# Kernel optimization log

Measured on AMD Instinct MI355X. Metric: run time of the kernel, lower is better.

## Reference

```python
import jax, jax.numpy as jnp
import numpy as np

D = 512
SCALE = 1.0 / np.sqrt(D).astype(np.float32)


def setup_inputs() -> dict:
    key = jax.random.key(0)
    ks = jax.random.split(key, 6)
    B, S = 8, 2048
    x = jax.random.normal(ks[0], (B, S, D), dtype=jnp.float32)
    bias = jax.random.normal(ks[1], (1,), dtype=jnp.float32)
    key_padding_mask = jax.random.randint(ks[2], (B, S), 0, 2).astype(jnp.bool_)
    # nn.Linear weights, stored as [out, in]; y = x @ W.T
    Wq = jax.random.normal(ks[3], (D, D), dtype=jnp.float32) * (1.0 / np.sqrt(D))
    Wk = jax.random.normal(ks[4], (D, D), dtype=jnp.float32) * (1.0 / np.sqrt(D))
    Wv = jax.random.normal(ks[5], (D, D), dtype=jnp.float32) * (1.0 / np.sqrt(D))
    return {"x": x, "bias": bias, "key_padding_mask": key_padding_mask,
            "Wq": Wq, "Wk": Wk, "Wv": Wv}


def reference(x, bias, key_padding_mask, Wq, Wk, Wv):
    # Projections (Linear without bias): [B,S,D] @ [D,D]^T
    Q = jnp.einsum('bsd,ed->bse', x, Wq)
    K = jnp.einsum('bsd,ed->bse', x, Wk)
    V = jnp.einsum('bsd,ed->bse', x, Wv)
    # Scaled scores with additive scalar bias: [B,S,S]
    scores = jnp.einsum('bqd,bkd->bqk', Q, K) * SCALE + bias
    # Key padding mask: mask keys (last dim) with -inf
    scores = jnp.where(key_padding_mask[:, None, :], -jnp.inf, scores)
    attn = jax.nn.softmax(scores, axis=-1)
    attn = jnp.nan_to_num(attn, nan=0.0)  # fully-masked rows -> 0
    # Dropout is inference no-op
    return jnp.einsum('bqk,bkd->bqd', attn, V)
```

## Files before the change

### kernel.cpp

```cpp
#include <hip/hip_runtime.h>

typedef short bf16x8 __attribute__((ext_vector_type(8)));
typedef float f32x4 __attribute__((ext_vector_type(4)));
typedef float f32x16 __attribute__((ext_vector_type(16)));

__device__ __forceinline__ ushort f2bf(float f) {
    union { float f; unsigned u; } v; v.f = f;
    unsigned r = (v.u + 0x7fffu + ((v.u >> 16) & 1u)) >> 16;
    return (ushort)r;
}
__device__ __forceinline__ float bf2f(ushort u) {
    union { unsigned u; float f; } v; v.u = ((unsigned)u) << 16;
    return v.f;
}
__device__ __forceinline__ void async_copy16(void* lds, const void* g) {
    __builtin_amdgcn_global_load_lds(
        (const __attribute__((address_space(1))) unsigned*)g,
        (__attribute__((address_space(3))) unsigned*)lds, 16, 0, 0);
}
__device__ __forceinline__ void lds_barrier() {
    asm volatile("s_waitcnt lgkmcnt(0)\n\ts_barrier" ::: "memory");
}

__global__ __launch_bounds__(256)
void prep_kernel(const float* __restrict__ x, const float* __restrict__ Wq,
                 const float* __restrict__ Wk, const float* __restrict__ Wv,
                 const int* __restrict__ mask,
                 ushort* __restrict__ xb, ushort* __restrict__ wqT,
                 ushort* __restrict__ wkT, ushort* __restrict__ wvb,
                 int* __restrict__ idx, int* __restrict__ cnt)
{
    const int bid = blockIdx.x, t = threadIdx.x;
    if (bid < 8192) {
        int i = (bid * 256 + t) * 4;
        float4 v = *(const float4*)(x + i);
        ushort4 o;
        o.x = f2bf(v.x); o.y = f2bf(v.y); o.z = f2bf(v.z); o.w = f2bf(v.w);
        *(ushort4*)(xb + i) = o;
    } else if (bid < 8320) {
        __shared__ ushort T[64][72];
        int r = bid - 8192;
        const int z = r >> 6; r &= 63;
        const float* in = z ? Wk : Wq;
        ushort* out     = z ? wkT : wqT;
        const int r0 = (r >> 3) * 64, c0 = (r & 7) * 64;
        const int rr = t >> 3, cc8 = (t & 7) * 8;
        #pragma unroll
        for (int pass = 0; pass < 2; ++pass) {
            int rw = rr + pass * 32;
            float4 a = *(const float4*)(in + (size_t)(r0 + rw) * 512 + c0 + cc8);
            float4 bq = *(const float4*)(in + (size_t)(r0 + rw) * 512 + c0 + cc8 + 4);
            T[rw][cc8+0]=f2bf(a.x);  T[rw][cc8+1]=f2bf(a.y);  T[rw][cc8+2]=f2bf(a.z);  T[rw][cc8+3]=f2bf(a.w);
            T[rw][cc8+4]=f2bf(bq.x); T[rw][cc8+5]=f2bf(bq.y); T[rw][cc8+6]=f2bf(bq.z); T[rw][cc8+7]=f2bf(bq.w);
        }
        __syncthreads();
        const int c = t >> 2, seg = (t & 3) * 16;
        ushort tmp[16];
        #pragma unroll
        for (int j = 0; j < 16; ++j) tmp[j] = T[seg + j][c];
        *(uint4*)(out + (size_t)(c0 + c) * 512 + r0 + seg)     = *(uint4*)&tmp[0];
        *(uint4*)(out + (size_t)(c0 + c) * 512 + r0 + seg + 8) = *(uint4*)&tmp[8];
    } else if (bid < 8576) {
        int i = ((bid - 8320) * 256 + t) * 4;
        float4 v = *(const float4*)(Wv + i);
        ushort4 o;
        o.x = f2bf(v.x); o.y = f2bf(v.y); o.z = f2bf(v.z); o.w = f2bf(v.w);
        *(ushort4*)(wvb + i) = o;
    } else {
        __shared__ int sc[256];
        int seg = bid - 8576, b = seg >> 1, half = seg & 1;
        const int* m = mask + b * 2048 + half * 1024;
        int v0 = (m[t*4+0] == 0), v1 = (m[t*4+1] == 0);
        int v2 = (m[t*4+2] == 0), v3 = (m[t*4+3] == 0);
        int c = v0 + v1 + v2 + v3;
        sc[t] = c; __syncthreads();
        for (int ofs = 1; ofs < 256; ofs <<= 1) {
            int xx = (t >= ofs) ? sc[t - ofs] : 0;
            __syncthreads(); sc[t] += xx; __syncthreads();
        }
        int pos = sc[t] - c + seg * 1024;
        if (v0) idx[pos++] = t*4+0;
        if (v1) idx[pos++] = t*4+1;
        if (v2) idx[pos++] = t*4+2;
        if (v3) idx[pos++] = t*4+3;
        if (t == 255) cnt[seg] = sc[255];
    }
}

__global__ __launch_bounds__(256)
void gather_cvt(const float* __restrict__ x, const int* __restrict__ idx,
                const int* __restrict__ cnt, ushort* __restrict__ xc)
{
    int seg = blockIdx.x, b = seg >> 1, half = seg & 1;
    int n = cnt[seg];
    int wave = threadIdx.x >> 6, lane = threadIdx.x & 63;
    int j0 = blockIdx.y * 64 + wave * 16;
    for (int i = 0; i < 16; ++i) {
        int j = j0 + i;
        uint4 val = {0u, 0u, 0u, 0u};
        if (j < n) {
            int src = idx[seg * 1024 + j];
            const float* r = x + ((size_t)(b * 2048 + half * 1024 + src)) * 512 + lane * 8;
            float4 a = *(const float4*)r, c4 = *(const float4*)(r + 4);
            ushort tmp[8];
            tmp[0]=f2bf(a.x); tmp[1]=f2bf(a.y); tmp[2]=f2bf(a.z); tmp[3]=f2bf(a.w);
            tmp[4]=f2bf(c4.x); tmp[5]=f2bf(c4.y); tmp[6]=f2bf(c4.z); tmp[7]=f2bf(c4.w);
            val = *(uint4*)tmp;
        }
        *(uint4*)(xc + ((size_t)(seg * 1024 + j)) * 512 + lane * 8) = val;
    }
}

__device__ __forceinline__ void gemm_core(const ushort* __restrict__ A,
                                          const ushort* __restrict__ B,
                                          ushort* __restrict__ C,
                                          int N, int K, int mBase, int nBase)
{
    __shared__ ushort As[128][32];
    __shared__ ushort Bs[128][32];
    const int tid = threadIdx.x;
    const int lane = tid & 63, wave = tid >> 6;
    const int wm = wave >> 1, wn = wave & 1;
    const int lr = lane & 15, lq = lane >> 4;
    const int sr = lane >> 2;
    const int sc = (lane & 3) * 8;

    f32x4 acc[4][4];
    #pragma unroll
    for (int i = 0; i < 4; ++i)
        #pragma unroll
        for (int j = 0; j < 4; ++j) acc[i][j] = (f32x4){0.f, 0.f, 0.f, 0.f};

    for (int k0 = 0; k0 < K; k0 += 32) {
        __syncthreads();
        #pragma unroll
        for (int j = 0; j < 2; ++j) {
            int rbase = wave * 32 + j * 16;
            async_copy16(&As[rbase][0], A + (size_t)(mBase + rbase + sr) * K + k0 + sc);
            async_copy16(&Bs[rbase][0], B + (size_t)(nBase + rbase + sr) * K + k0 + sc);
        }
        __syncthreads();
        bf16x8 af[4], bfr[4];
        #pragma unroll
        for (int mi = 0; mi < 4; ++mi) af[mi] = *(const bf16x8*)&As[wm * 64 + mi * 16 + lr][lq * 8];
        #pragma unroll
        for (int ni = 0; ni < 4; ++ni) bfr[ni] = *(const bf16x8*)&Bs[wn * 64 + ni * 16 + lr][lq * 8];
        #pragma unroll
        for (int mi = 0; mi < 4; ++mi)
            #pragma unroll
            for (int ni = 0; ni < 4; ++ni)
                acc[mi][ni] = __builtin_amdgcn_mfma_f32_16x16x32_bf16(af[mi], bfr[ni], acc[mi][ni], 0, 0, 0);
    }
    #pragma unroll
    for (int mi = 0; mi < 4; ++mi)
        #pragma unroll
        for (int ni = 0; ni < 4; ++ni)
            #pragma unroll
            for (int r = 0; r < 4; ++r) {
                int m = mBase + wm * 64 + mi * 16 + lq * 4 + r;
                int n = nBase + wn * 64 + ni * 16 + lr;
                C[(size_t)m * N + n] = f2bf(acc[mi][ni][r]);
            }
}

__global__ __launch_bounds__(256, 2)
void gemm_m(const ushort* __restrict__ A, const ushort* __restrict__ B,
            ushort* __restrict__ C) {
    gemm_core(A, B, C, 512, 512, blockIdx.y * 128, blockIdx.x * 128);
}

__global__ __launch_bounds__(256, 2)
void gemm_kv(const ushort* __restrict__ xc, const ushort* __restrict__ Mb,
             ushort* __restrict__ Kc, const ushort* __restrict__ wv,
             ushort* __restrict__ Vtc, const int* __restrict__ cnt)
{
    const ushort *A, *B; ushort* C; int N, mBase, nBase;
    if (blockIdx.z == 0) {
        mBase = blockIdx.y * 128; nBase = blockIdx.x * 128;
        if ((mBase & 1023) >= cnt[mBase >> 10]) return;
        A = xc; B = Mb; C = Kc; N = 512;
    } else {
        mBase = blockIdx.x * 128; nBase = blockIdx.y * 128;
        if ((nBase & 1023) >= cnt[nBase >> 10]) return;
        A = wv; B = xc; C = Vtc; N = 16384;
    }
    gemm_core(A, B, C, N, 512, mBase, nBase);
}

__global__ __launch_bounds__(256, 2)
void attn_kernel(const ushort* __restrict__ Qg, const ushort* __restrict__ Kcg,
                 const ushort* __restrict__ Vtcg, const int* __restrict__ cntg,
                 ushort* __restrict__ Pog, float* __restrict__ Mlg)
{
    const int S = 2048;
    const float SL2E = 0.0637587160f;

    __shared__ ushort Ks[32][548];
    __shared__ ushort Vs[512][36];
    __shared__ ushort Ps[2][32][36];

    const int lin = blockIdx.x + 32 * blockIdx.y + 256 * blockIdx.z;
    const int seg = (lin & 7) * 2 + (lin >> 8);
    const int qt  = (lin >> 3) & 31;
    const int b = seg >> 1, half = seg & 1;

    const int tid = threadIdx.x, lane = tid & 63, wave = tid >> 6;
    const int lr = lane & 15, lq = lane >> 4;
    const int p = wave >> 1, s = wave & 1;
    const int l32 = lane & 31, lh = lane >> 5;

    const int n = cntg[seg];
    const int ntiles = (n + 31) >> 5;

    const ushort* Qp = Qg + ((size_t)b * S + qt * 64 + wave * 16 + lr) * 512;
    bf16x8 qf[16];
    #pragma unroll
    for (int c = 0; c < 16; ++c) qf[c] = *(const bf16x8*)(Qp + c * 32 + lq * 8);

    f32x16 o[8];
    #pragma unroll
    for (int i = 0; i < 8; ++i)
        #pragma unroll
        for (int r = 0; r < 16; ++r) o[i][r] = 0.f;
    float l_i[4] = {0.f, 0.f, 0.f, 0.f};

    const char* Kseg = (const char*)(Kcg + (size_t)seg * 1024 * 512);
    const char* Vseg = (const char*)Vtcg + (size_t)(seg * 1024) * 2;

    {
        #pragma unroll
        for (int i = 0; i < 8; ++i) {
            int row = wave * 8 + i;
            async_copy16(&Ks[row][0], Kseg + (size_t)row * 1024 + lane * 16);
        }
    }

    for (int kt = 0; kt < ntiles; ++kt) {
        const int key0 = kt * 32;
        __syncthreads();
        uint4 vreg[8];
        {
            const char* gV = Vseg + (size_t)key0 * 2;
            #pragma unroll
            for (int i = 0; i < 8; ++i) {
                int off = i * 4096 + tid * 16;
                vreg[i] = *(const uint4*)(gV + (size_t)(off >> 6) * 32768 + (off & 63));
            }
        }
        const bool va0 = (key0 + lr) < n;
        const bool va1 = (key0 + 16 + lr) < n;
        f32x4 sA = (f32x4){0.f,0.f,0.f,0.f}, sB = (f32x4){0.f,0.f,0.f,0.f};
        f32x4 sC = (f32x4){0.f,0.f,0.f,0.f}, sD = (f32x4){0.f,0.f,0.f,0.f};
        __builtin_amdgcn_s_setprio(1);
        #pragma unroll
        for (int ks = 0; ks < 16; ks += 2) {
            bf16x8 kf0a = *(const bf16x8*)&Ks[lr][ks * 32 + lq * 8];
            bf16x8 kf1a = *(const bf16x8*)&Ks[16 + lr][ks * 32 + lq * 8];
            bf16x8 kf0b = *(const bf16x8*)&Ks[lr][(ks + 1) * 32 + lq * 8];
            bf16x8 kf1b = *(const bf16x8*)&Ks[16 + lr][(ks + 1) * 32 + lq * 8];
            sA = __builtin_amdgcn_mfma_f32_16x16x32_bf16(qf[ks], kf0a, sA, 0, 0, 0);
            sB = __builtin_amdgcn_mfma_f32_16x16x32_bf16(qf[ks], kf1a, sB, 0, 0, 0);
            sC = __builtin_amdgcn_mfma_f32_16x16x32_bf16(qf[ks + 1], kf0b, sC, 0, 0, 0);
            sD = __builtin_amdgcn_mfma_f32_16x16x32_bf16(qf[ks + 1], kf1b, sD, 0, 0, 0);
        }
        __builtin_amdgcn_s_setprio(0);
        #pragma unroll
        for (int r = 0; r < 4; ++r) {
            float s0 = sA[r] + sC[r], s1 = sB[r] + sD[r];
            float p0 = va0 ? exp2f(fmaf(s0, SL2E, -8.f)) : 0.f;
            float p1 = va1 ? exp2f(fmaf(s1, SL2E, -8.f)) : 0.f;
            l_i[r] += p0 + p1;
            Ps[p][16 * s + lq * 4 + r][lr]      = f2bf(p0);
            Ps[p][16 * s + lq * 4 + r][16 + lr] = f2bf(p1);
        }
        #pragma unroll
        for (int i = 0; i < 8; ++i) {
            int off = i * 4096 + tid * 16;
            int row = off >> 6, col = off & 63;
            *(uint4*)((char*)Vs + row * 72 + col) = vreg[i];
        }
        lds_barrier();
        if (kt + 1 < ntiles) {
            const char* gK = Kseg + (size_t)(key0 + 32) * 1024;
            #pragma unroll
            for (int i = 0; i < 8; ++i) {
                int row = wave * 8 + i;
                async_copy16(&Ks[row][0], gK + (size_t)row * 1024 + lane * 16);
            }
        }
        bf16x8 pA0 = *(const bf16x8*)&Ps[p][l32][lh * 8];
        bf16x8 pA1 = *(const bf16x8*)&Ps[p][l32][16 + lh * 8];
        __builtin_amdgcn_s_setprio(1);
        #pragma unroll
        for (int dt = 0; dt < 8; ++dt) {
            int d = s * 256 + dt * 32 + l32;
            bf16x8 v0 = *(const bf16x8*)&Vs[d][lh * 8];
            bf16x8 v1 = *(const bf16x8*)&Vs[d][16 + lh * 8];
            o[dt] = __builtin_amdgcn_mfma_f32_32x32x16_bf16(pA0, v0, o[dt], 0, 0, 0);
            o[dt] = __builtin_amdgcn_mfma_f32_32x32x16_bf16(pA1, v1, o[dt], 0, 0, 0);
        }
        __builtin_amdgcn_s_setprio(0);
    }
    #pragma unroll
    for (int r = 0; r < 4; ++r)
        #pragma unroll
        for (int off = 1; off < 16; off <<= 1)
            l_i[r] += __shfl_xor(l_i[r], off, 16);
    const size_t growbase = (size_t)half * 16384 + (size_t)b * S + qt * 64;
    if (lr == 0) {
        #pragma unroll
        for (int r = 0; r < 4; ++r)
            Mlg[growbase + wave * 16 + lq * 4 + r] = l_i[r];
    }
    ushort* Pop = Pog + (growbase + p * 32) * 512;
    #pragma unroll
    for (int dt = 0; dt < 8; ++dt) {
        int ocol = s * 256 + dt * 32 + l32;
        #pragma unroll
        for (int r = 0; r < 16; ++r) {
            int orow = (r & 3) + 8 * (r >> 2) + 4 * lh;
            Pop[(size_t)orow * 512 + ocol] = f2bf(o[dt][r]);
        }
    }
}

__global__ __launch_bounds__(256)
void combine_kernel(const ushort* __restrict__ Po, const float* __restrict__ Ml,
                    float* __restrict__ out)
{
    int i = (blockIdx.x * 256 + threadIdx.x) * 4;
    int row = i >> 9;
    float l = Ml[row] + Ml[16384 + row];
    float s = l > 0.f ? 1.f / l : 0.f;
    ushort4 p1 = *(const ushort4*)(Po + i);
    ushort4 p2 = *(const ushort4*)(Po + 8388608 + i);
    float4 o;
    o.x = (bf2f(p1.x) + bf2f(p2.x)) * s;
    o.y = (bf2f(p1.y) + bf2f(p2.y)) * s;
    o.z = (bf2f(p1.z) + bf2f(p2.z)) * s;
    o.w = (bf2f(p1.w) + bf2f(p2.w)) * s;
    *(float4*)(out + i) = o;
}

extern "C" void kernel_launch(void* const* d_in, const int* in_sizes, int n_in,
                              void* d_out, int out_size, void* d_ws, size_t ws_size,
                              hipStream_t stream) {
    const float* x  = (const float*)d_in[0];
    const int* mask = (const int*)d_in[2];
    const float* Wq = (const float*)d_in[3];
    const float* Wk = (const float*)d_in[4];
    const float* Wv = (const float*)d_in[5];
    float* out = (float*)d_out;

    ushort* ws   = (ushort*)d_ws;
    ushort* xb   = ws;
    ushort* wqT  = ws + 8388608;
    ushort* wkT  = wqT + 262144;
    ushort* wvb  = wkT + 262144;
    ushort* xc   = ws + 9175040;
    ushort* Pob  = ws + 9175040;
    ushort* Mb   = ws + 17563648;
    int*    idxb = (int*)(ws + 17825792);
    ushort* Kc   = ws + 25952256;
    ushort* Vtc  = ws + 34340864;
    float*  Mlb  = (float*)(ws + 42729472);
    int*    cntb = (int*)(ws + 42795008);

    prep_kernel<<<8592, 256, 0, stream>>>(x, Wq, Wk, Wv, mask,
                                          xb, wqT, wkT, wvb, idxb, cntb);
    gather_cvt<<<dim3(16, 16), 256, 0, stream>>>(x, idxb, cntb, xc);
    gemm_m<<<dim3(4, 4), 256, 0, stream>>>(wqT, wkT, Mb);
    gemm_kv<<<dim3(4, 128, 2), 256, 0, stream>>>(xc, Mb, Kc, wvb, Vtc, cntb);
    attn_kernel<<<dim3(32, 8, 2), 256, 0, stream>>>(xb, Kc, Vtc, cntb, Pob, Mlb);
    combine_kernel<<<8192, 256, 0, stream>>>(Pob, Mlb, out);
}
```

Before: 228.5 us.

## Pre-tile V into MFMA fragment layout and read it from global in attention

The V-projection GEMM now writes its output in a tiled layout that matches the 32x32x16 MFMA B-operand fragments. This lets the attention kernel load V fragments directly from global memory instead of staging them through an LDS buffer. The attention key tile grows from 32 to 64 keys per iteration, which halves the barriers and loop overhead, and K staging is enlarged to match. The gather step now copies the already-converted bf16 x instead of reloading fp32 and converting again. In exchange, V reads no longer get LDS reuse across waves, so they depend on cache hit rates, and the GEMM epilogue stores become scattered.

```diff
diff --git a/kernel.cpp b/kernel.cpp
--- a/kernel.cpp
+++ b/kernel.cpp
@@ -88,7 +88,7 @@
 }
 
 __global__ __launch_bounds__(256)
-void gather_cvt(const float* __restrict__ x, const int* __restrict__ idx,
+void gather_cvt(const ushort* __restrict__ xb, const int* __restrict__ idx,
                 const int* __restrict__ cnt, ushort* __restrict__ xc)
 {
     int seg = blockIdx.x, b = seg >> 1, half = seg & 1;
@@ -100,12 +100,7 @@
         uint4 val = {0u, 0u, 0u, 0u};
         if (j < n) {
             int src = idx[seg * 1024 + j];
-            const float* r = x + ((size_t)(b * 2048 + half * 1024 + src)) * 512 + lane * 8;
-            float4 a = *(const float4*)r, c4 = *(const float4*)(r + 4);
-            ushort tmp[8];
-            tmp[0]=f2bf(a.x); tmp[1]=f2bf(a.y); tmp[2]=f2bf(a.z); tmp[3]=f2bf(a.w);
-            tmp[4]=f2bf(c4.x); tmp[5]=f2bf(c4.y); tmp[6]=f2bf(c4.z); tmp[7]=f2bf(c4.w);
-            val = *(uint4*)tmp;
+            val = *(const uint4*)(xb + ((size_t)(b * 2048 + half * 1024 + src)) * 512 + lane * 8);
         }
         *(uint4*)(xc + ((size_t)(seg * 1024 + j)) * 512 + lane * 8) = val;
     }
@@ -114,7 +109,8 @@
 __device__ __forceinline__ void gemm_core(const ushort* __restrict__ A,
                                           const ushort* __restrict__ B,
                                           ushort* __restrict__ C,
-                                          int N, int K, int mBase, int nBase)
+                                          int N, int K, int mBase, int nBase,
+                                          int vt_mode)
 {
     __shared__ ushort As[128][32];
     __shared__ ushort Bs[128][32];
@@ -159,14 +155,22 @@
             for (int r = 0; r < 4; ++r) {
                 int m = mBase + wm * 64 + mi * 16 + lq * 4 + r;
                 int n = nBase + wn * 64 + ni * 16 + lr;
-                C[(size_t)m * N + n] = f2bf(acc[mi][ni][r]);
+                if (!vt_mode) {
+                    C[(size_t)m * N + n] = f2bf(acc[mi][ni][r]);
+                } else {
+                    int sseg = n >> 10, key = n & 1023;
+                    size_t ix = (size_t)sseg * 524288 + (size_t)(key >> 5) * 16384
+                              + (size_t)(m >> 5) * 1024 + ((key >> 4) & 1) * 512
+                              + (m & 31) * 16 + (key & 15);
+                    C[ix] = f2bf(acc[mi][ni][r]);
+                }
             }
 }
 
 __global__ __launch_bounds__(256, 2)
 void gemm_m(const ushort* __restrict__ A, const ushort* __restrict__ B,
             ushort* __restrict__ C) {
-    gemm_core(A, B, C, 512, 512, blockIdx.y * 128, blockIdx.x * 128);
+    gemm_core(A, B, C, 512, 512, blockIdx.y * 128, blockIdx.x * 128, 0);
 }
 
 __global__ __launch_bounds__(256, 2)
@@ -174,17 +178,15 @@
              ushort* __restrict__ Kc, const ushort* __restrict__ wv,
              ushort* __restrict__ Vtc, const int* __restrict__ cnt)
 {
-    const ushort *A, *B; ushort* C; int N, mBase, nBase;
     if (blockIdx.z == 0) {
-        mBase = blockIdx.y * 128; nBase = blockIdx.x * 128;
+        int mBase = blockIdx.y * 128, nBase = blockIdx.x * 128;
         if ((mBase & 1023) >= cnt[mBase >> 10]) return;
-        A = xc; B = Mb; C = Kc; N = 512;
+        gemm_core(xc, Mb, Kc, 512, 512, mBase, nBase, 0);
     } else {
-        mBase = blockIdx.x * 128; nBase = blockIdx.y * 128;
+        int mBase = blockIdx.x * 128, nBase = blockIdx.y * 128;
         if ((nBase & 1023) >= cnt[nBase >> 10]) return;
-        A = wv; B = xc; C = Vtc; N = 16384;
-    }
-    gemm_core(A, B, C, N, 512, mBase, nBase);
+        gemm_core(wv, xc, Vtc, 16384, 512, mBase, nBase, 1);
+    }
 }
 
 __global__ __launch_bounds__(256, 2)
@@ -195,9 +197,8 @@
     const int S = 2048;
     const float SL2E = 0.0637587160f;
 
-    __shared__ ushort Ks[32][548];
-    __shared__ ushort Vs[512][36];
-    __shared__ ushort Ps[2][32][36];
+    __shared__ ushort Ks[64][548];
+    __shared__ ushort Ps[2][32][68];
 
     const int lin = blockIdx.x + 32 * blockIdx.y + 256 * blockIdx.z;
     const int seg = (lin & 7) * 2 + (lin >> 8);
@@ -210,7 +211,7 @@
     const int l32 = lane & 31, lh = lane >> 5;
 
     const int n = cntg[seg];
-    const int ntiles = (n + 31) >> 5;
+    const int ntiles = (n + 63) >> 6;
 
     const ushort* Qp = Qg + ((size_t)b * S + qt * 64 + wave * 16 + lr) * 512;
     bf16x8 qf[16];
@@ -225,81 +226,77 @@
     float l_i[4] = {0.f, 0.f, 0.f, 0.f};
 
     const char* Kseg = (const char*)(Kcg + (size_t)seg * 1024 * 512);
-    const char* Vseg = (const char*)Vtcg + (size_t)(seg * 1024) * 2;
-
-    {
-        #pragma unroll
-        for (int i = 0; i < 8; ++i) {
-            int row = wave * 8 + i;
+    const char* Vseg = (const char*)(Vtcg + (size_t)seg * 524288);
+
+    if (ntiles > 0) {
+        #pragma unroll
+        for (int i = 0; i < 16; ++i) {
+            int row = wave * 16 + i;
             async_copy16(&Ks[row][0], Kseg + (size_t)row * 1024 + lane * 16);
         }
-    }
-
-    for (int kt = 0; kt < ntiles; ++kt) {
-        const int key0 = kt * 32;
-        __syncthreads();
-        uint4 vreg[8];
-        {
-            const char* gV = Vseg + (size_t)key0 * 2;
-            #pragma unroll
-            for (int i = 0; i < 8; ++i) {
-                int off = i * 4096 + tid * 16;
-                vreg[i] = *(const uint4*)(gV + (size_t)(off >> 6) * 32768 + (off & 63));
-            }
-        }
-        const bool va0 = (key0 + lr) < n;
-        const bool va1 = (key0 + 16 + lr) < n;
-        f32x4 sA = (f32x4){0.f,0.f,0.f,0.f}, sB = (f32x4){0.f,0.f,0.f,0.f};
-        f32x4 sC = (f32x4){0.f,0.f,0.f,0.f}, sD = (f32x4){0.f,0.f,0.f,0.f};
-        __builtin_amdgcn_s_setprio(1);
-        #pragma unroll
-        for (int ks = 0; ks < 16; ks += 2) {
-            bf16x8 kf0a = *(const bf16x8*)&Ks[lr][ks * 32 + lq * 8];
-            bf16x8 kf1a = *(const bf16x8*)&Ks[16 + lr][ks * 32 + lq * 8];
-            bf16x8 kf0b = *(const bf16x8*)&Ks[lr][(ks + 1) * 32 + lq * 8];
-            bf16x8 kf1b = *(const bf16x8*)&Ks[16 + lr][(ks + 1) * 32 + lq * 8];
-            sA = __builtin_amdgcn_mfma_f32_16x16x32_bf16(qf[ks], kf0a, sA, 0, 0, 0);
-            sB = __builtin_amdgcn_mfma_f32_16x16x32_bf16(qf[ks], kf1a, sB, 0, 0, 0);
-            sC = __builtin_amdgcn_mfma_f32_16x16x32_bf16(qf[ks + 1], kf0b, sC, 0, 0, 0);
-            sD = __builtin_amdgcn_mfma_f32_16x16x32_bf16(qf[ks + 1], kf1b, sD, 0, 0, 0);
-        }
-        __builtin_amdgcn_s_setprio(0);
-        #pragma unroll
-        for (int r = 0; r < 4; ++r) {
-            float s0 = sA[r] + sC[r], s1 = sB[r] + sD[r];
-            float p0 = va0 ? exp2f(fmaf(s0, SL2E, -8.f)) : 0.f;
-            float p1 = va1 ? exp2f(fmaf(s1, SL2E, -8.f)) : 0.f;
-            l_i[r] += p0 + p1;
-            Ps[p][16 * s + lq * 4 + r][lr]      = f2bf(p0);
-            Ps[p][16 * s + lq * 4 + r][16 + lr] = f2bf(p1);
-        }
-        #pragma unroll
-        for (int i = 0; i < 8; ++i) {
-            int off = i * 4096 + tid * 16;
-            int row = off >> 6, col = off & 63;
-            *(uint4*)((char*)Vs + row * 72 + col) = vreg[i];
-        }
-        lds_barrier();
-        if (kt + 1 < ntiles) {
-            const char* gK = Kseg + (size_t)(key0 + 32) * 1024;
-            #pragma unroll
-            for (int i = 0; i < 8; ++i) {
-                int row = wave * 8 + i;
-                async_copy16(&Ks[row][0], gK + (size_t)row * 1024 + lane * 16);
-            }
-        }
-        bf16x8 pA0 = *(const bf16x8*)&Ps[p][l32][lh * 8];
-        bf16x8 pA1 = *(const bf16x8*)&Ps[p][l32][16 + lh * 8];
-        __builtin_amdgcn_s_setprio(1);
-        #pragma unroll
-        for (int dt = 0; dt < 8; ++dt) {
-            int d = s * 256 + dt * 32 + l32;
-            bf16x8 v0 = *(const bf16x8*)&Vs[d][lh * 8];
-            bf16x8 v1 = *(const bf16x8*)&Vs[d][16 + lh * 8];
-            o[dt] = __builtin_amdgcn_mfma_f32_32x32x16_bf16(pA0, v0, o[dt], 0, 0, 0);
-            o[dt] = __builtin_amdgcn_mfma_f32_32x32x16_bf16(pA1, v1, o[dt], 0, 0, 0);
-        }
-        __builtin_amdgcn_s_setprio(0);
+
+        for (int kt = 0; kt < ntiles; ++kt) {
+            const int key0 = kt * 64;
+            __syncthreads();
+            f32x4 sf[4][2];
+            #pragma unroll
+            for (int g = 0; g < 4; ++g) {
+                sf[g][0] = (f32x4){0.f,0.f,0.f,0.f};
+                sf[g][1] = (f32x4){0.f,0.f,0.f,0.f};
+            }
+            __builtin_amdgcn_s_setprio(1);
+            #pragma unroll
+            for (int ks = 0; ks < 16; ks += 2) {
+                #pragma unroll
+                for (int g = 0; g < 4; ++g) {
+                    bf16x8 kfa = *(const bf16x8*)&Ks[g * 16 + lr][ks * 32 + lq * 8];
+                    bf16x8 kfb = *(const bf16x8*)&Ks[g * 16 + lr][(ks + 1) * 32 + lq * 8];
+                    sf[g][0] = __builtin_amdgcn_mfma_f32_16x16x32_bf16(qf[ks], kfa, sf[g][0], 0, 0, 0);
+                    sf[g][1] = __builtin_amdgcn_mfma_f32_16x16x32_bf16(qf[ks + 1], kfb, sf[g][1], 0, 0, 0);
+                }
+            }
+            __builtin_amdgcn_s_setprio(0);
+            #pragma unroll
+            for (int r = 0; r < 4; ++r) {
+                float acc = 0.f;
+                #pragma unroll
+                for (int g = 0; g < 4; ++g) {
+                    bool va = (key0 + g * 16 + lr) < n;
+                    float pv = va ? exp2f(fmaf(sf[g][0][r] + sf[g][1][r], SL2E, -8.f)) : 0.f;
+                    acc += pv;
+                    Ps[p][16 * s + lq * 4 + r][g * 16 + lr] = f2bf(pv);
+                }
+                l_i[r] += acc;
+            }
+            lds_barrier();
+            if (kt + 1 < ntiles) {
+                const char* gK = Kseg + (size_t)(key0 + 64) * 1024;
+                #pragma unroll
+                for (int i = 0; i < 16; ++i) {
+                    int row = wave * 16 + i;
+                    async_copy16(&Ks[row][0], gK + (size_t)row * 1024 + lane * 16);
+                }
+            }
+            bf16x8 pA[4];
+            #pragma unroll
+            for (int g = 0; g < 4; ++g)
+                pA[g] = *(const bf16x8*)&Ps[p][l32][g * 16 + lh * 8];
+            __builtin_amdgcn_s_setprio(1);
+            #pragma unroll
+            for (int dt = 0; dt < 8; ++dt) {
+                const int db = s * 8 + dt;
+                #pragma unroll
+                for (int g = 0; g < 4; ++g) {
+                    const int kt32 = (key0 >> 5) + (g >> 1);
+                    const char* a = Vseg
+                        + ((size_t)kt32 * 16384 + (size_t)db * 1024 + (g & 1) * 512) * 2
+                        + l32 * 32 + lh * 16;
+                    bf16x8 v = *(const bf16x8*)a;
+                    o[dt] = __builtin_amdgcn_mfma_f32_32x32x16_bf16(pA[g], v, o[dt], 0, 0, 0);
+                }
+            }
+            __builtin_amdgcn_s_setprio(0);
+        }
     }
     #pragma unroll
     for (int r = 0; r < 4; ++r)
@@ -368,7 +365,7 @@
 
     prep_kernel<<<8592, 256, 0, stream>>>(x, Wq, Wk, Wv, mask,
                                           xb, wqT, wkT, wvb, idxb, cntb);
-    gather_cvt<<<dim3(16, 16), 256, 0, stream>>>(x, idxb, cntb, xc);
+    gather_cvt<<<dim3(16, 16), 256, 0, stream>>>(xb, idxb, cntb, xc);
     gemm_m<<<dim3(4, 4), 256, 0, stream>>>(wqT, wkT, Mb);
     gemm_kv<<<dim3(4, 128, 2), 256, 0, stream>>>(xc, Mb, Kc, wvb, Vtc, cntb);
     attn_kernel<<<dim3(32, 8, 2), 256, 0, stream>>>(xb, Kc, Vtc, cntb, Pob, Mlb);
```

Measured after the change: 272.6 us. 19.3% more time.
